# Kernel tuning notes

Measured on AMD Instinct MI355X. Metric: run time of the kernel, lower is better.

The kernel has to match this reference:

```python
import jax, jax.numpy as jnp
import numpy as np

B, IN_DIM = 1024, 128
MBD_IN, MBD_OUT, MBD_K = 64, 50, 5
BN_EPS = 1e-5


def setup_inputs() -> dict:
    key = jax.random.key(0)
    ks = jax.random.split(key, 16)
    n = lambda k, s: jax.random.normal(k, s, dtype=jnp.float32)
    return {
        "x": n(ks[0], (B, IN_DIM)),
        # MLP: 128->256->128(BN)->64, LeakyReLU(0.2)
        "W1": n(ks[1], (IN_DIM, 256)) * 0.05, "b1": jnp.zeros((256,), jnp.float32),
        "W2": n(ks[2], (256, 128)) * 0.05, "b2": jnp.zeros((128,), jnp.float32),
        "gamma": jnp.ones((128,), jnp.float32), "beta": jnp.zeros((128,), jnp.float32),
        "W3": n(ks[3], (128, 64)) * 0.05, "b3": jnp.zeros((64,), jnp.float32),
        # SelfAttention1D(64, heads=1) on a length-1 token: softmax over a single
        # key is identically 1, so output = residual + out_proj(value_proj(h)).
        # Wq/Wk provably do not affect the output and are omitted.
        "Wv": n(ks[4], (64, 64)) * 0.05, "bv": jnp.zeros((64,), jnp.float32),
        "Wo": n(ks[5], (64, 64)) * 0.05, "bo": jnp.zeros((64,), jnp.float32),
        # MinibatchDiscrimination tensor T: [64, 50, 5], init 0.05*randn as in source
        "T": n(ks[6], (MBD_IN, MBD_OUT, MBD_K)) * 0.05,
        "Ws": n(ks[7], (MBD_IN + MBD_OUT, 1)) * 0.05, "bs": jnp.zeros((1,), jnp.float32),
    }


def _lrelu(h):
    return jnp.where(h > 0, h, 0.2 * h)


def reference(x, W1, b1, W2, b2, gamma, beta, W3, b3, Wv, bv, Wo, bo, T, Ws, bs):
    # --- MLP backbone (BatchNorm1d in training mode: batch statistics) ---
    h = _lrelu(x @ W1 + b1)                      # [B,256]
    h = h @ W2 + b2                              # [B,128]
    mu = h.mean(axis=0)
    var = ((h - mu) ** 2).mean(axis=0)           # biased variance (torch BN)
    h = (h - mu) * jax.lax.rsqrt(var + BN_EPS) * gamma + beta
    h = _lrelu(h)
    h = _lrelu(h @ W3 + b3)                      # [B,64]
    # --- SelfAttention1D, seq_len=1 -> attn weights == 1 ---
    h = h + (h @ Wv + bv) @ Wo + bo              # [B,64]
    # --- Minibatch discrimination: fused all-pairs L1 + exp-sum ---
    M = (h @ T.reshape(MBD_IN, MBD_OUT * MBD_K)).reshape(-1, MBD_OUT, MBD_K)  # [B,50,5]
    diff = jnp.abs(M[:, None, :, :] - M[None, :, :, :]).sum(-1)               # [B,B,50]
    o = jnp.exp(-diff).sum(axis=0) - 1.0          # [B,50] (self term exp(0)=1 removed)
    feat = jnp.concatenate([h, o], axis=1)        # [B,114]
    score = (feat @ Ws + bs).squeeze(-1)          # [B]
    return score
```

## Files before the change

kernel.cpp:

```cpp
#include <hip/hip_runtime.h>
#include <math.h>

#define LRELU(v) ((v) > 0.f ? (v) : 0.2f * (v))

__global__ __launch_bounds__(256) void k1_mlp12(
    const float* __restrict__ x,
    const float* __restrict__ W1, const float* __restrict__ b1,
    const float* __restrict__ W2, const float* __restrict__ b2,
    float* __restrict__ h2g, float* __restrict__ stats)
{
    __shared__ float xs[256];
    __shared__ float h1s[512];
    __shared__ float ssum[256];
    __shared__ float ssq[256];
    const int t = threadIdx.x;
    const int r0 = blockIdx.x * 2;

    xs[t] = x[r0 * 128 + t];
    __syncthreads();

    {
        float a0 = b1[t], a1 = a0;
        for (int k = 0; k < 128; ++k) {
            float w = W1[k * 256 + t];
            a0 += xs[k] * w;
            a1 += xs[128 + k] * w;
        }
        h1s[t] = LRELU(a0);
        h1s[256 + t] = LRELU(a1);
    }
    __syncthreads();

    {
        const int c = t & 127;
        const int rr = t >> 7;
        float a = b2[c];
        for (int k = 0; k < 256; ++k)
            a += h1s[rr * 256 + k] * W2[k * 128 + c];
        h2g[(r0 + rr) * 128 + c] = a;
        ssum[t] = a;
        ssq[t] = a * a;
    }
    __syncthreads();
    if (t < 128)      atomicAdd(stats + t, ssum[t] + ssum[128 + t]);
    else { int c = t - 128; atomicAdd(stats + 128 + c, ssq[c] + ssq[128 + c]); }
}

__global__ __launch_bounds__(256) void k2_bn_attn_m(
    const float* __restrict__ h2g, const float* __restrict__ stats,
    const float* __restrict__ gamma, const float* __restrict__ beta,
    const float* __restrict__ W3, const float* __restrict__ b3,
    const float* __restrict__ Wv, const float* __restrict__ bv,
    const float* __restrict__ Wo, const float* __restrict__ bo,
    const float* __restrict__ T2,
    float* __restrict__ h4g, float* __restrict__ Mt)
{
    __shared__ float a[256];
    __shared__ float h3s[128];
    __shared__ float vss[128];
    __shared__ float h4s[128];
    const int t = threadIdx.x;
    const int r0 = blockIdx.x * 2;

    {
        const int c = t & 127;
        float s = stats[c], ss = stats[128 + c];
        float mean = s * (1.f / 1024.f);
        float var = ss * (1.f / 1024.f) - mean * mean;
        float rstd = rsqrtf(var + 1e-5f);
        float v = (h2g[r0 * 128 + t] - mean) * rstd * gamma[c] + beta[c];
        a[t] = LRELU(v);
    }
    __syncthreads();

    const int row = t >> 6, col = t & 63;
    if (t < 128) {
        float acc = b3[col];
        for (int k = 0; k < 128; ++k) acc += a[row * 128 + k] * W3[k * 64 + col];
        h3s[row * 64 + col] = LRELU(acc);
    }
    __syncthreads();
    if (t < 128) {
        float acc = bv[col];
        for (int k = 0; k < 64; ++k) acc += h3s[row * 64 + k] * Wv[k * 64 + col];
        vss[row * 64 + col] = acc;
    }
    __syncthreads();
    if (t < 128) {
        float acc = bo[col];
        for (int k = 0; k < 64; ++k) acc += vss[row * 64 + k] * Wo[k * 64 + col];
        float h4 = h3s[row * 64 + col] + acc;
        h4s[row * 64 + col] = h4;
        h4g[(r0 + row) * 64 + col] = h4;
    }
    __syncthreads();

    if (t < 250) {
        float m0 = 0.f, m1 = 0.f;
        for (int k = 0; k < 64; ++k) {
            float w = T2[k * 250 + t];
            m0 += h4s[k] * w;
            m1 += h4s[64 + k] * w;
        }
        Mt[(size_t)t * 1024 + r0]     = m0;
        Mt[(size_t)t * 1024 + r0 + 1] = m1;
    } else {
        Mt[(size_t)t * 1024 + r0]     = 0.f;
        Mt[(size_t)t * 1024 + r0 + 1] = 0.f;
    }
    if (t < 4) {
        Mt[(size_t)(256 + t) * 1024 + r0]     = 0.f;
        Mt[(size_t)(256 + t) * 1024 + r0 + 1] = 0.f;
    }
}

__global__ __launch_bounds__(256) void k3_pairs(
    const float* __restrict__ Mt, float* __restrict__ opart)
{
    __shared__ float mi[2560];
    const int t = threadIdx.x;
    const int b = blockIdx.x;
    const int jt = b / 104;
    const int rem = b - jt * 104;
    const int ct = rem >> 3;
    const int ic = rem & 7;
    const int jl = t & 63, cl = t >> 6;
    const int j = jt * 64 + jl;
    const int c = ct * 4 + cl;
    const int i0 = ic * 128;

    for (int qq = 0; qq < 10; ++qq) {
        int idx = qq * 256 + t;
        int cc = idx >> 7, il = idx & 127;
        mi[idx] = Mt[(size_t)(ct * 20 + cc) * 1024 + i0 + il];
    }

    float mj0 = Mt[(size_t)(c * 5 + 0) * 1024 + j];
    float mj1 = Mt[(size_t)(c * 5 + 1) * 1024 + j];
    float mj2 = Mt[(size_t)(c * 5 + 2) * 1024 + j];
    float mj3 = Mt[(size_t)(c * 5 + 3) * 1024 + j];
    float mj4 = Mt[(size_t)(c * 5 + 4) * 1024 + j];
    __syncthreads();

    const float4* m0 = (const float4*)(mi + (cl * 5 + 0) * 128);
    const float4* m1 = (const float4*)(mi + (cl * 5 + 1) * 128);
    const float4* m2 = (const float4*)(mi + (cl * 5 + 2) * 128);
    const float4* m3 = (const float4*)(mi + (cl * 5 + 3) * 128);
    const float4* m4 = (const float4*)(mi + (cl * 5 + 4) * 128);

    float acc0 = 0.f, acc1 = 0.f, acc2 = 0.f, acc3 = 0.f;
    for (int p = 0; p < 32; ++p) {
        float4 v0 = m0[p], v1 = m1[p], v2 = m2[p], v3 = m3[p], v4 = m4[p];
        float d0 = fabsf(v0.x - mj0) + fabsf(v1.x - mj1) + fabsf(v2.x - mj2)
                 + fabsf(v3.x - mj3) + fabsf(v4.x - mj4);
        float d1 = fabsf(v0.y - mj0) + fabsf(v1.y - mj1) + fabsf(v2.y - mj2)
                 + fabsf(v3.y - mj3) + fabsf(v4.y - mj4);
        float d2 = fabsf(v0.z - mj0) + fabsf(v1.z - mj1) + fabsf(v2.z - mj2)
                 + fabsf(v3.z - mj3) + fabsf(v4.z - mj4);
        float d3 = fabsf(v0.w - mj0) + fabsf(v1.w - mj1) + fabsf(v2.w - mj2)
                 + fabsf(v3.w - mj3) + fabsf(v4.w - mj4);
        acc0 += __expf(-d0);
        acc1 += __expf(-d1);
        acc2 += __expf(-d2);
        acc3 += __expf(-d3);
    }
    opart[(size_t)(ic * 1024 + j) * 52 + c] = (acc0 + acc1) + (acc2 + acc3);
}

__global__ __launch_bounds__(64) void k4_score(
    const float* __restrict__ h4g, const float* __restrict__ opart,
    const float* __restrict__ Ws, const float* __restrict__ bs,
    float* __restrict__ out)
{
    const int j = blockIdx.x, t = threadIdx.x;
    float contrib = h4g[j * 64 + t] * Ws[t];
    if (t < 50) {
        float s = 0.f;
        for (int ic = 0; ic < 8; ++ic)
            s += opart[(size_t)(ic * 1024 + j) * 52 + t];
        contrib += (s - 1.0f) * Ws[64 + t];
    }
    for (int off = 32; off > 0; off >>= 1)
        contrib += __shfl_down(contrib, off, 64);
    if (t == 0) out[j] = contrib + bs[0];
}

extern "C" void kernel_launch(void* const* d_in, const int* in_sizes, int n_in,
                              void* d_out, int out_size, void* d_ws, size_t ws_size,
                              hipStream_t stream)
{
    const float* x     = (const float*)d_in[0];
    const float* W1    = (const float*)d_in[1];
    const float* b1    = (const float*)d_in[2];
    const float* W2    = (const float*)d_in[3];
    const float* b2    = (const float*)d_in[4];
    const float* gamma = (const float*)d_in[5];
    const float* beta  = (const float*)d_in[6];
    const float* W3    = (const float*)d_in[7];
    const float* b3    = (const float*)d_in[8];
    const float* Wv    = (const float*)d_in[9];
    const float* bv    = (const float*)d_in[10];
    const float* Wo    = (const float*)d_in[11];
    const float* bo    = (const float*)d_in[12];
    const float* T2    = (const float*)d_in[13];
    const float* Ws    = (const float*)d_in[14];
    const float* bs    = (const float*)d_in[15];

    float* ws    = (float*)d_ws;
    float* h2    = ws + 0;
    float* stats = ws + 131072;
    float* h4    = ws + 131328;
    float* Mt    = ws + 196864;
    float* opart = ws + 463104;
    float* out   = (float*)d_out;

    hipMemsetAsync(stats, 0, 256 * sizeof(float), stream);
    hipLaunchKernelGGL(k1_mlp12, dim3(512), dim3(256), 0, stream,
                       x, W1, b1, W2, b2, h2, stats);
    hipLaunchKernelGGL(k2_bn_attn_m, dim3(512), dim3(256), 0, stream,
                       h2, stats, gamma, beta, W3, b3, Wv, bv, Wo, bo, T2, h4, Mt);
    hipLaunchKernelGGL(k3_pairs, dim3(1664), dim3(256), 0, stream, Mt, opart);
    hipLaunchKernelGGL(k4_score, dim3(1024), dim3(64), 0, stream,
                       h4, opart, Ws, bs, out);
}
```

Before: 140.3 us.

## Fuse score reduction into pair kernel via atomics and use exp2 with prescaled M

```diff
diff --git a/kernel.cpp b/kernel.cpp
--- a/kernel.cpp
+++ b/kernel.cpp
@@ -2,6 +2,7 @@
 #include <math.h>
 
 #define LRELU(v) ((v) > 0.f ? (v) : 0.2f * (v))
+#define LOG2E 1.44269504088896340736f
 
 __global__ __launch_bounds__(256) void k1_mlp12(
     const float* __restrict__ x,
@@ -53,12 +54,14 @@
     const float* __restrict__ Wv, const float* __restrict__ bv,
     const float* __restrict__ Wo, const float* __restrict__ bo,
     const float* __restrict__ T2,
-    float* __restrict__ h4g, float* __restrict__ Mt)
+    const float* __restrict__ Wsc, const float* __restrict__ bs,
+    float* __restrict__ Mt, float* __restrict__ score)
 {
     __shared__ float a[256];
     __shared__ float h3s[128];
     __shared__ float vss[128];
     __shared__ float h4s[128];
+    __shared__ float red[4];
     const int t = threadIdx.x;
     const int r0 = blockIdx.x * 2;
 
@@ -89,9 +92,7 @@
     if (t < 128) {
         float acc = bo[col];
         for (int k = 0; k < 64; ++k) acc += vss[row * 64 + k] * Wo[k * 64 + col];
-        float h4 = h3s[row * 64 + col] + acc;
-        h4s[row * 64 + col] = h4;
-        h4g[(r0 + row) * 64 + col] = h4;
+        h4s[row * 64 + col] = h3s[row * 64 + col] + acc;
     }
     __syncthreads();
 
@@ -102,8 +103,8 @@
             m0 += h4s[k] * w;
             m1 += h4s[64 + k] * w;
         }
-        Mt[(size_t)t * 1024 + r0]     = m0;
-        Mt[(size_t)t * 1024 + r0 + 1] = m1;
+        Mt[(size_t)t * 1024 + r0]     = m0 * LOG2E;
+        Mt[(size_t)t * 1024 + r0 + 1] = m1 * LOG2E;
     } else {
         Mt[(size_t)t * 1024 + r0]     = 0.f;
         Mt[(size_t)t * 1024 + r0 + 1] = 0.f;
@@ -112,12 +113,23 @@
         Mt[(size_t)(256 + t) * 1024 + r0]     = 0.f;
         Mt[(size_t)(256 + t) * 1024 + r0 + 1] = 0.f;
     }
+
+    float contrib = 0.f;
+    if (t < 128)            contrib = h4s[t] * Wsc[col];
+    else if (t < 192) { int c2 = t & 63; contrib = (c2 < 50) ? Wsc[64 + c2] : 0.f; }
+    for (int off = 32; off > 0; off >>= 1)
+        contrib += __shfl_down(contrib, off, 64);
+    if ((t & 63) == 0) red[t >> 6] = contrib;
+    __syncthreads();
+    if (t < 2) score[r0 + t] = red[t] + bs[0] - red[2];
 }
 
 __global__ __launch_bounds__(256) void k3_pairs(
-    const float* __restrict__ Mt, float* __restrict__ opart)
+    const float* __restrict__ Mt, const float* __restrict__ Wsc,
+    float* __restrict__ score)
 {
     __shared__ float mi[2560];
+    __shared__ float sred[256];
     const int t = threadIdx.x;
     const int b = blockIdx.x;
     const int jt = b / 104;
@@ -129,10 +141,11 @@
     const int c = ct * 4 + cl;
     const int i0 = ic * 128;
 
-    for (int qq = 0; qq < 10; ++qq) {
+    for (int qq = 0; qq < 5; ++qq) {
         int idx = qq * 256 + t;
-        int cc = idx >> 7, il = idx & 127;
-        mi[idx] = Mt[(size_t)(ct * 20 + cc) * 1024 + i0 + il];
+        int cc = idx >> 6, il = idx & 63;
+        *(float2*)(mi + cc * 128 + il * 2) =
+            *(const float2*)(Mt + (size_t)(ct * 20 + cc) * 1024 + i0 + il * 2);
     }
 
     float mj0 = Mt[(size_t)(c * 5 + 0) * 1024 + j];
@@ -159,30 +172,18 @@
                  + fabsf(v3.z - mj3) + fabsf(v4.z - mj4);
         float d3 = fabsf(v0.w - mj0) + fabsf(v1.w - mj1) + fabsf(v2.w - mj2)
                  + fabsf(v3.w - mj3) + fabsf(v4.w - mj4);
-        acc0 += __expf(-d0);
-        acc1 += __expf(-d1);
-        acc2 += __expf(-d2);
-        acc3 += __expf(-d3);
-    }
-    opart[(size_t)(ic * 1024 + j) * 52 + c] = (acc0 + acc1) + (acc2 + acc3);
-}
-
-__global__ __launch_bounds__(64) void k4_score(
-    const float* __restrict__ h4g, const float* __restrict__ opart,
-    const float* __restrict__ Ws, const float* __restrict__ bs,
-    float* __restrict__ out)
-{
-    const int j = blockIdx.x, t = threadIdx.x;
-    float contrib = h4g[j * 64 + t] * Ws[t];
-    if (t < 50) {
-        float s = 0.f;
-        for (int ic = 0; ic < 8; ++ic)
-            s += opart[(size_t)(ic * 1024 + j) * 52 + t];
-        contrib += (s - 1.0f) * Ws[64 + t];
-    }
-    for (int off = 32; off > 0; off >>= 1)
-        contrib += __shfl_down(contrib, off, 64);
-    if (t == 0) out[j] = contrib + bs[0];
+        acc0 += exp2f(-d0);
+        acc1 += exp2f(-d1);
+        acc2 += exp2f(-d2);
+        acc3 += exp2f(-d3);
+    }
+    float w = (c < 50) ? Wsc[64 + c] : 0.f;
+    sred[t] = ((acc0 + acc1) + (acc2 + acc3)) * w;
+    __syncthreads();
+    if (t < 64) {
+        float s = (sred[t] + sred[64 + t]) + (sred[128 + t] + sred[192 + t]);
+        atomicAdd(score + jt * 64 + t, s);
+    }
 }
 
 extern "C" void kernel_launch(void* const* d_in, const int* in_sizes, int n_in,
@@ -209,17 +210,14 @@
     float* ws    = (float*)d_ws;
     float* h2    = ws + 0;
     float* stats = ws + 131072;
-    float* h4    = ws + 131328;
-    float* Mt    = ws + 196864;
-    float* opart = ws + 463104;
+    float* Mt    = ws + 131328;
     float* out   = (float*)d_out;
 
     hipMemsetAsync(stats, 0, 256 * sizeof(float), stream);
     hipLaunchKernelGGL(k1_mlp12, dim3(512), dim3(256), 0, stream,
                        x, W1, b1, W2, b2, h2, stats);
     hipLaunchKernelGGL(k2_bn_attn_m, dim3(512), dim3(256), 0, stream,
-                       h2, stats, gamma, beta, W3, b3, Wv, bv, Wo, bo, T2, h4, Mt);
-    hipLaunchKernelGGL(k3_pairs, dim3(1664), dim3(256), 0, stream, Mt, opart);
-    hipLaunchKernelGGL(k4_score, dim3(1024), dim3(64), 0, stream,
-                       h4, opart, Ws, bs, out);
-}
+                       h2, stats, gamma, beta, W3, b3, Wv, bv, Wo, bo, T2,
+                       Ws, bs, Mt, out);
+    hipLaunchKernelGGL(k3_pairs, dim3(1664), dim3(256), 0, stream, Mt, Ws, out);
+}
```

After: 144.6 us. 1.03x slower.
